# Kernel optimization log

Hardware: AMD Instinct MI355X
Metric: run time of the kernel (lower is better)

## Reference

```python
import jax, jax.numpy as jnp
import numpy as np

TEMPERATURE = 4.0

def setup_inputs() -> dict:
    key = jax.random.key(0)
    k1, k2 = jax.random.split(key)
    query = jax.random.normal(k1, (128, 128, 256), dtype=jnp.float32)      # (B, D, Q)
    context = jax.random.normal(k2, (128, 128, 32, 32), dtype=jnp.float32)  # (B, D, H, W)
    return {"query": query, "context": context}

def reference(query, context):
    B, D, Q = query.shape
    H, W = context.shape[2], context.shape[3]
    L = H * W  # context_length
    context_flat = context.reshape(B, D, L)                    # (B, D, L)
    # scores[b, l, q] = sum_d context[b, d, l] * query[b, d, q]
    scores = jnp.einsum('bdl,bdq->blq', context_flat, query)   # (B, L, Q)
    # first softmax: over query dim (context -> query)
    attn_q = jax.nn.softmax(scores, axis=-1)                   # (B, L, Q)
    # second softmax: over context dim with temperature (query -> context)
    attn_c = jax.nn.softmax(attn_q.transpose(0, 2, 1) * TEMPERATURE, axis=-1)  # (B, Q, L)
    # weighted_context[b, d, q] = sum_l context[b, d, l] * attn_c[b, q, l]
    weighted_context = jnp.einsum('bdl,bql->bdq', context_flat, attn_c)  # (B, D, Q)
    attention_map = attn_c.reshape(B, Q, H, W)
    return (weighted_context, attention_map)
```

## Files before the change

kernel.cpp:

```cpp
#include <hip/hip_runtime.h>
#include <math.h>

#define B_ 128
#define D_ 128
#define Q_ 256
#define L_ 1024

typedef __attribute__((ext_vector_type(8))) short s16x8;
typedef __attribute__((ext_vector_type(4))) float f32x4;

__device__ __forceinline__ unsigned short f2bf(float x) {
  unsigned u = __float_as_uint(x);
  u += 0x7FFF + ((u >> 16) & 1);
  return (unsigned short)(u >> 16);
}
__device__ __forceinline__ float bf2f(unsigned short h) {
  return __uint_as_float(((unsigned)h) << 16);
}
__device__ __forceinline__ uint2 pack4bf(float4 v) {
  uint2 r;
  r.x = ((unsigned)f2bf(v.y) << 16) | (unsigned)f2bf(v.x);
  r.y = ((unsigned)f2bf(v.w) << 16) | (unsigned)f2bf(v.z);
  return r;
}
__device__ __forceinline__ void split8(const float* x, s16x8& hi, s16x8& lo) {
#pragma unroll
  for (int j = 0; j < 8; j++) {
    unsigned short h = f2bf(x[j]);
    hi[j] = (short)h;
    lo[j] = (short)f2bf(x[j] - bf2f(h));
  }
}

__global__ __launch_bounds__(256, 2) void k1_attnq(
    const float* __restrict__ query, const float* __restrict__ ctx,
    float* __restrict__ attq, float* __restrict__ pd) {
  __shared__ float sm[4][64], ss[4][64], fm[64], fs[64];
  const int lt = blockIdx.x, b = blockIdx.y;
  const int l0 = lt * 64;
  const int tid = threadIdx.x;
  const int wq = tid >> 6;
  const int lane = tid & 63, quad = lane >> 4, l15 = lane & 15;

  const float* Qb = query + (size_t)b * D_ * Q_;
  const float* Cb = ctx + (size_t)b * D_ * L_ + l0;

  f32x4 acc[4][4];
#pragma unroll
  for (int mi = 0; mi < 4; mi++)
#pragma unroll
    for (int ni = 0; ni < 4; ni++) acc[mi][ni] = (f32x4){0.f, 0.f, 0.f, 0.f};

#pragma unroll 2
  for (int k0 = 0; k0 < D_; k0 += 32) {
    const int kq = k0 + quad * 8;
    s16x8 ah[4], al[4], bh[4], bl[4];
#pragma unroll
    for (int mi = 0; mi < 4; mi++) {
      const float* p = Qb + (size_t)kq * Q_ + wq * 64 + mi * 16 + l15;
      float x[8];
#pragma unroll
      for (int j = 0; j < 8; j++) x[j] = p[(size_t)j * Q_];
      split8(x, ah[mi], al[mi]);
    }
#pragma unroll
    for (int ni = 0; ni < 4; ni++) {
      const float* p = Cb + (size_t)kq * L_ + ni * 16 + l15;
      float x[8];
#pragma unroll
      for (int j = 0; j < 8; j++) x[j] = p[(size_t)j * L_];
      split8(x, bh[ni], bl[ni]);
    }
#pragma unroll
    for (int mi = 0; mi < 4; mi++)
#pragma unroll
      for (int ni = 0; ni < 4; ni++) {
        acc[mi][ni] = __builtin_amdgcn_mfma_f32_16x16x32_bf16(
            ah[mi], bh[ni], acc[mi][ni], 0, 0, 0);
        acc[mi][ni] = __builtin_amdgcn_mfma_f32_16x16x32_bf16(
            ah[mi], bl[ni], acc[mi][ni], 0, 0, 0);
        acc[mi][ni] = __builtin_amdgcn_mfma_f32_16x16x32_bf16(
            al[mi], bh[ni], acc[mi][ni], 0, 0, 0);
      }
  }

#pragma unroll
  for (int ni = 0; ni < 4; ni++) {
    float m = -1e30f;
#pragma unroll
    for (int mi = 0; mi < 4; mi++)
#pragma unroll
      for (int r = 0; r < 4; r++) m = fmaxf(m, acc[mi][ni][r]);
    m = fmaxf(m, __shfl_xor(m, 16));
    m = fmaxf(m, __shfl_xor(m, 32));
    float s = 0.f;
#pragma unroll
    for (int mi = 0; mi < 4; mi++)
#pragma unroll
      for (int r = 0; r < 4; r++) s += __expf(acc[mi][ni][r] - m);
    s += __shfl_xor(s, 16);
    s += __shfl_xor(s, 32);
    if (quad == 0) {
      sm[wq][ni * 16 + l15] = m;
      ss[wq][ni * 16 + l15] = s;
    }
  }
  __syncthreads();
  if (tid < 64) {
    float m0 = sm[0][tid], m1 = sm[1][tid], m2 = sm[2][tid], m3 = sm[3][tid];
    float M = fmaxf(fmaxf(m0, m1), fmaxf(m2, m3));
    float S = ss[0][tid] * __expf(m0 - M) + ss[1][tid] * __expf(m1 - M) +
              ss[2][tid] * __expf(m2 - M) + ss[3][tid] * __expf(m3 - M);
    fm[tid] = M;
    fs[tid] = 1.f / S;
  }
  __syncthreads();

  float fmv[4], fiv[4];
#pragma unroll
  for (int ni = 0; ni < 4; ni++) {
    fmv[ni] = fm[ni * 16 + l15];
    fiv[ni] = fs[ni * 16 + l15];
  }
  float* Ab = attq + ((size_t)b * Q_ + wq * 64) * L_ + l0;
  float dsum[4][4];
#pragma unroll
  for (int mi = 0; mi < 4; mi++)
#pragma unroll
    for (int r = 0; r < 4; r++) dsum[mi][r] = 0.f;
#pragma unroll
  for (int mi = 0; mi < 4; mi++)
#pragma unroll
    for (int r = 0; r < 4; r++) {
      const int q = mi * 16 + quad * 4 + r;
#pragma unroll
      for (int ni = 0; ni < 4; ni++) {
        float a = __expf(acc[mi][ni][r] - fmv[ni]) * fiv[ni];
        Ab[(size_t)q * L_ + ni * 16 + l15] = a;
        dsum[mi][r] += __expf(4.f * a);
      }
    }
#pragma unroll
  for (int mi = 0; mi < 4; mi++)
#pragma unroll
    for (int r = 0; r < 4; r++) {
      float v = dsum[mi][r];
      v += __shfl_xor(v, 1);
      v += __shfl_xor(v, 2);
      v += __shfl_xor(v, 4);
      v += __shfl_xor(v, 8);
      dsum[mi][r] = v;
    }
  if (l15 == 0) {
#pragma unroll
    for (int mi = 0; mi < 4; mi++)
#pragma unroll
      for (int r = 0; r < 4; r++)
        pd[(size_t)lt * (B_ * Q_) + b * Q_ + wq * 64 + mi * 16 + quad * 4 +
           r] = dsum[mi][r];
  }
}

__global__ __launch_bounds__(256) void k2_invd(const float* __restrict__ pd,
                                               float* __restrict__ invd) {
  const int i = blockIdx.x * 256 + threadIdx.x;
  float s = 0.f;
#pragma unroll
  for (int t = 0; t < 16; t++) s += pd[(size_t)t * (B_ * Q_) + i];
  invd[i] = 1.f / s;
}

__global__ __launch_bounds__(256) void k4_weighted(
    const float* __restrict__ ctx, float* __restrict__ attn,
    const float* __restrict__ invd, float* __restrict__ W) {
  __shared__ unsigned short As[128][32];
  __shared__ unsigned short Bs[64][32];
  const int b = blockIdx.y, q0 = blockIdx.x * 64;
  const int tid = threadIdx.x;
  const int w = tid >> 6, lane = tid & 63, quad = lane >> 4, l15 = lane & 15;
  const int wd = (w >> 1) * 64, wn = (w & 1) * 32;

  const float* Cb = ctx + (size_t)b * D_ * L_;
  float* Ab = attn + ((size_t)b * Q_ + q0) * L_;

  const int lc = (tid & 7) * 4;
  const int rr = tid >> 3;
  const float id0 = invd[b * Q_ + q0 + rr];
  const float id1 = invd[b * Q_ + q0 + rr + 32];

  f32x4 acc[4][2];
#pragma unroll
  for (int mi = 0; mi < 4; mi++)
#pragma unroll
    for (int ni = 0; ni < 2; ni++) acc[mi][ni] = (f32x4){0.f, 0.f, 0.f, 0.f};

  for (int l0 = 0; l0 < L_; l0 += 32) {
    if (l0) __syncthreads();
#pragma unroll
    for (int h = 0; h < 4; h++) {
      const int d = rr + h * 32;
      float4 cv = *(const float4*)(Cb + (size_t)d * L_ + l0 + lc);
      *(uint2*)&As[d][lc] = pack4bf(cv);
    }
#pragma unroll
    for (int h = 0; h < 2; h++) {
      const int q = rr + h * 32;
      float* p = Ab + (size_t)q * L_ + l0 + lc;
      float4 a = *(const float4*)p;
      const float idv = h ? id1 : id0;
      float4 t;
      t.x = __expf(4.f * a.x) * idv;
      t.y = __expf(4.f * a.y) * idv;
      t.z = __expf(4.f * a.z) * idv;
      t.w = __expf(4.f * a.w) * idv;
      *(float4*)p = t;
      *(uint2*)&Bs[q][lc] = pack4bf(t);
    }
    __syncthreads();

    s16x8 af[4], bq[2];
#pragma unroll
    for (int mi = 0; mi < 4; mi++)
      af[mi] = *(const s16x8*)&As[wd + mi * 16 + l15][quad * 8];
#pragma unroll
    for (int ni = 0; ni < 2; ni++)
      bq[ni] = *(const s16x8*)&Bs[wn + ni * 16 + l15][quad * 8];
#pragma unroll
    for (int mi = 0; mi < 4; mi++)
#pragma unroll
      for (int ni = 0; ni < 2; ni++)
        acc[mi][ni] = __builtin_amdgcn_mfma_f32_16x16x32_bf16(
            af[mi], bq[ni], acc[mi][ni], 0, 0, 0);
  }

  float* Wb = W + (size_t)b * D_ * Q_;
#pragma unroll
  for (int mi = 0; mi < 4; mi++)
#pragma unroll
    for (int ni = 0; ni < 2; ni++)
#pragma unroll
      for (int r = 0; r < 4; r++)
        Wb[(size_t)(wd + mi * 16 + quad * 4 + r) * Q_ + q0 + wn + ni * 16 +
           l15] = acc[mi][ni][r];
}

extern "C" void kernel_launch(void* const* d_in, const int* in_sizes, int n_in,
                              void* d_out, int out_size, void* d_ws,
                              size_t ws_size, hipStream_t stream) {
  const float* query = (const float*)d_in[0];
  const float* ctx = (const float*)d_in[1];
  float* W = (float*)d_out;
  float* attn = (float*)d_out + (size_t)B_ * D_ * Q_;

  const size_t need = (size_t)17 * B_ * Q_ * sizeof(float);
  float* pd = (ws_size >= need && d_ws) ? (float*)d_ws : W;
  float* invd = pd + (size_t)16 * B_ * Q_;

  k1_attnq<<<dim3(L_ / 64, B_), 256, 0, stream>>>(query, ctx, attn, pd);
  k2_invd<<<dim3(B_ * Q_ / 256), 256, 0, stream>>>(pd, invd);
  k4_weighted<<<dim3(Q_ / 64, B_), 256, 0, stream>>>(ctx, attn, invd, W);
}
```

Measured before the change: 316.8 us.

## Pre-split inputs to bf16 hi/lo layout and store intermediate attention in fp16

Adds a pre-pass that transposes query and context into K-contiguous bf16 hi/lo arrays, staged in the output buffers. The score kernel can then load MFMA fragments with vector loads instead of strided scalar loads and skip the per-block split. The first-softmax result now goes to an fp16 workspace instead of an fp32 read-modify-write of the attention map, which reduces traffic in the weighted-sum kernel. The trade-offs are an extra launch, a large workspace requirement that falls back to the old path if unmet, and lower precision in the intermediate attention values.

```diff
diff --git a/kernel.cpp b/kernel.cpp
--- a/kernel.cpp
+++ b/kernel.cpp
@@ -5,9 +5,12 @@
 #define D_ 128
 #define Q_ 256
 #define L_ 1024
+#define BQ_ ((size_t)B_ * Q_)
+#define BQL_ ((size_t)B_ * Q_ * L_)
 
 typedef __attribute__((ext_vector_type(8))) short s16x8;
 typedef __attribute__((ext_vector_type(4))) float f32x4;
+typedef __attribute__((ext_vector_type(8))) _Float16 f16x8;
 
 __device__ __forceinline__ unsigned short f2bf(float x) {
   unsigned u = __float_as_uint(x);
@@ -32,7 +35,189 @@
   }
 }
 
-__global__ __launch_bounds__(256, 2) void k1_attnq(
+__global__ __launch_bounds__(256) void p1_split(
+    const float* __restrict__ query, const float* __restrict__ ctx,
+    unsigned short* __restrict__ Qs, unsigned short* __restrict__ Cs) {
+  __shared__ float T[128][132];
+  const int b = blockIdx.y;
+  const int xt = blockIdx.x;
+  const float* src;
+  unsigned short* dst;
+  int C, c0;
+  if (xt < 2) {
+    src = query + (size_t)b * D_ * Q_;
+    dst = Qs + (size_t)b * Q_ * 256;
+    C = Q_;
+    c0 = xt * 128;
+  } else {
+    src = ctx + (size_t)b * D_ * L_;
+    dst = Cs + (size_t)b * L_ * 256;
+    C = L_;
+    c0 = (xt - 2) * 128;
+  }
+  const int t = threadIdx.x;
+  const int col4 = (t & 31) * 4, kr = t >> 5;
+#pragma unroll
+  for (int i = 0; i < 16; i++) {
+    const int k = kr + i * 8;
+    *(float4*)&T[k][col4] = *(const float4*)(src + (size_t)k * C + c0 + col4);
+  }
+  __syncthreads();
+  const int q = t >> 1, half = t & 1;
+  unsigned short* drow = dst + (size_t)(c0 + q) * 256;
+#pragma unroll
+  for (int g = 0; g < 8; g++) {
+    const int k0 = half * 64 + g * 8;
+    float x[8];
+#pragma unroll
+    for (int j = 0; j < 8; j++) x[j] = T[k0 + j][q];
+    uint4 vh, vl;
+    unsigned hh[8], ll[8];
+#pragma unroll
+    for (int j = 0; j < 8; j++) {
+      unsigned short h = f2bf(x[j]);
+      hh[j] = h;
+      ll[j] = f2bf(x[j] - bf2f(h));
+    }
+    vh.x = hh[0] | (hh[1] << 16);
+    vh.y = hh[2] | (hh[3] << 16);
+    vh.z = hh[4] | (hh[5] << 16);
+    vh.w = hh[6] | (hh[7] << 16);
+    vl.x = ll[0] | (ll[1] << 16);
+    vl.y = ll[2] | (ll[3] << 16);
+    vl.z = ll[4] | (ll[5] << 16);
+    vl.w = ll[6] | (ll[7] << 16);
+    *(uint4*)&drow[k0] = vh;
+    *(uint4*)&drow[128 + k0] = vl;
+  }
+}
+
+template <bool F16>
+__global__ __launch_bounds__(256) void k1_fast(
+    const unsigned short* __restrict__ Qs, const unsigned short* __restrict__ Cs,
+    void* __restrict__ attq, float* __restrict__ pd) {
+  __shared__ float sm[4][64], ss[4][64], fm[64], fs[64];
+  const int lt = blockIdx.x, b = blockIdx.y;
+  const int l0 = lt * 64;
+  const int tid = threadIdx.x;
+  const int wq = tid >> 6;
+  const int lane = tid & 63, quad = lane >> 4, l15 = lane & 15;
+
+  const unsigned short* Qb = Qs + (size_t)b * Q_ * 256;
+  const unsigned short* Cb = Cs + (size_t)b * L_ * 256;
+
+  f32x4 acc[4][4];
+#pragma unroll
+  for (int mi = 0; mi < 4; mi++)
+#pragma unroll
+    for (int ni = 0; ni < 4; ni++) acc[mi][ni] = (f32x4){0.f, 0.f, 0.f, 0.f};
+
+#pragma unroll 2
+  for (int k0 = 0; k0 < D_; k0 += 32) {
+    s16x8 ah[4], al[4], bh[4], bl[4];
+#pragma unroll
+    for (int mi = 0; mi < 4; mi++) {
+      const unsigned short* p =
+          Qb + (size_t)(wq * 64 + mi * 16 + l15) * 256 + k0 + quad * 8;
+      ah[mi] = *(const s16x8*)p;
+      al[mi] = *(const s16x8*)(p + 128);
+    }
+#pragma unroll
+    for (int ni = 0; ni < 4; ni++) {
+      const unsigned short* p =
+          Cb + (size_t)(l0 + ni * 16 + l15) * 256 + k0 + quad * 8;
+      bh[ni] = *(const s16x8*)p;
+      bl[ni] = *(const s16x8*)(p + 128);
+    }
+#pragma unroll
+    for (int mi = 0; mi < 4; mi++)
+#pragma unroll
+      for (int ni = 0; ni < 4; ni++) {
+        acc[mi][ni] = __builtin_amdgcn_mfma_f32_16x16x32_bf16(
+            ah[mi], bh[ni], acc[mi][ni], 0, 0, 0);
+        acc[mi][ni] = __builtin_amdgcn_mfma_f32_16x16x32_bf16(
+            ah[mi], bl[ni], acc[mi][ni], 0, 0, 0);
+        acc[mi][ni] = __builtin_amdgcn_mfma_f32_16x16x32_bf16(
+            al[mi], bh[ni], acc[mi][ni], 0, 0, 0);
+      }
+  }
+
+#pragma unroll
+  for (int ni = 0; ni < 4; ni++) {
+    float m = -1e30f;
+#pragma unroll
+    for (int mi = 0; mi < 4; mi++)
+#pragma unroll
+      for (int r = 0; r < 4; r++) m = fmaxf(m, acc[mi][ni][r]);
+    m = fmaxf(m, __shfl_xor(m, 16));
+    m = fmaxf(m, __shfl_xor(m, 32));
+    float s = 0.f;
+#pragma unroll
+    for (int mi = 0; mi < 4; mi++)
+#pragma unroll
+      for (int r = 0; r < 4; r++) s += __expf(acc[mi][ni][r] - m);
+    s += __shfl_xor(s, 16);
+    s += __shfl_xor(s, 32);
+    if (quad == 0) {
+      sm[wq][ni * 16 + l15] = m;
+      ss[wq][ni * 16 + l15] = s;
+    }
+  }
+  __syncthreads();
+  if (tid < 64) {
+    float m0 = sm[0][tid], m1 = sm[1][tid], m2 = sm[2][tid], m3 = sm[3][tid];
+    float M = fmaxf(fmaxf(m0, m1), fmaxf(m2, m3));
+    float S = ss[0][tid] * __expf(m0 - M) + ss[1][tid] * __expf(m1 - M) +
+              ss[2][tid] * __expf(m2 - M) + ss[3][tid] * __expf(m3 - M);
+    fm[tid] = M;
+    fs[tid] = 1.f / S;
+  }
+  __syncthreads();
+
+  float fmv[4], fiv[4];
+#pragma unroll
+  for (int ni = 0; ni < 4; ni++) {
+    fmv[ni] = fm[ni * 16 + l15];
+    fiv[ni] = fs[ni * 16 + l15];
+  }
+  float dsum[4][4];
+#pragma unroll
+  for (int mi = 0; mi < 4; mi++)
+#pragma unroll
+    for (int r = 0; r < 4; r++) dsum[mi][r] = 0.f;
+
+  const size_t rowbase = ((size_t)b * Q_ + wq * 64) * L_ + l0;
+#pragma unroll
+  for (int mi = 0; mi < 4; mi++)
+#pragma unroll
+    for (int r = 0; r < 4; r++) {
+      const int q = mi * 16 + quad * 4 + r;
+#pragma unroll
+      for (int ni = 0; ni < 4; ni++) {
+        float a = __expf(acc[mi][ni][r] - fmv[ni]) * fiv[ni];
+        if (F16)
+          ((_Float16*)attq)[rowbase + (size_t)q * L_ + ni * 16 + l15] =
+              (_Float16)a;
+        else
+          ((float*)attq)[rowbase + (size_t)q * L_ + ni * 16 + l15] = a;
+        dsum[mi][r] += __expf(4.f * a);
+      }
+    }
+#pragma unroll
+  for (int mi = 0; mi < 4; mi++)
+#pragma unroll
+    for (int r = 0; r < 4; r++) {
+      float v = dsum[mi][r];
+      v += __shfl_xor(v, 1);
+      v += __shfl_xor(v, 2);
+      v += __shfl_xor(v, 4);
+      v += __shfl_xor(v, 8);
+      if (l15 == 0)
+        pd[(size_t)lt * BQ_ + b * Q_ + wq * 64 + mi * 16 + quad * 4 + r] = v;
+    }
+}
+
+__global__ __launch_bounds__(256, 2) void k1_slow(
     const float* __restrict__ query, const float* __restrict__ ctx,
     float* __restrict__ attq, float* __restrict__ pd) {
   __shared__ float sm[4][64], ss[4][64], fm[64], fs[64];
@@ -149,16 +334,9 @@
       v += __shfl_xor(v, 2);
       v += __shfl_xor(v, 4);
       v += __shfl_xor(v, 8);
-      dsum[mi][r] = v;
-    }
-  if (l15 == 0) {
-#pragma unroll
-    for (int mi = 0; mi < 4; mi++)
-#pragma unroll
-      for (int r = 0; r < 4; r++)
-        pd[(size_t)lt * (B_ * Q_) + b * Q_ + wq * 64 + mi * 16 + quad * 4 +
-           r] = dsum[mi][r];
-  }
+      if (l15 == 0)
+        pd[(size_t)lt * BQ_ + b * Q_ + wq * 64 + mi * 16 + quad * 4 + r] = v;
+    }
 }
 
 __global__ __launch_bounds__(256) void k2_invd(const float* __restrict__ pd,
@@ -166,13 +344,15 @@
   const int i = blockIdx.x * 256 + threadIdx.x;
   float s = 0.f;
 #pragma unroll
-  for (int t = 0; t < 16; t++) s += pd[(size_t)t * (B_ * Q_) + i];
+  for (int t = 0; t < 16; t++) s += pd[(size_t)t * BQ_ + i];
   invd[i] = 1.f / s;
 }
 
+template <bool F16>
 __global__ __launch_bounds__(256) void k4_weighted(
-    const float* __restrict__ ctx, float* __restrict__ attn,
-    const float* __restrict__ invd, float* __restrict__ W) {
+    const float* __restrict__ ctx, const void* __restrict__ attn,
+    float* __restrict__ map, const float* __restrict__ invd,
+    float* __restrict__ W) {
   __shared__ unsigned short As[128][32];
   __shared__ unsigned short Bs[64][32];
   const int b = blockIdx.y, q0 = blockIdx.x * 64;
@@ -181,12 +361,16 @@
   const int wd = (w >> 1) * 64, wn = (w & 1) * 32;
 
   const float* Cb = ctx + (size_t)b * D_ * L_;
-  float* Ab = attn + ((size_t)b * Q_ + q0) * L_;
-
-  const int lc = (tid & 7) * 4;
-  const int rr = tid >> 3;
-  const float id0 = invd[b * Q_ + q0 + rr];
-  const float id1 = invd[b * Q_ + q0 + rr + 32];
+  const int lc = (tid & 7) * 4, rr = tid >> 3;
+
+  const int qv = tid >> 2, lc8 = (tid & 3) * 8;
+  float idv = 0.f, id0 = 0.f, id1 = 0.f;
+  if (F16) {
+    idv = invd[b * Q_ + q0 + qv];
+  } else {
+    id0 = invd[b * Q_ + q0 + rr];
+    id1 = invd[b * Q_ + q0 + rr + 32];
+  }
 
   f32x4 acc[4][2];
 #pragma unroll
@@ -202,19 +386,37 @@
       float4 cv = *(const float4*)(Cb + (size_t)d * L_ + l0 + lc);
       *(uint2*)&As[d][lc] = pack4bf(cv);
     }
-#pragma unroll
-    for (int h = 0; h < 2; h++) {
-      const int q = rr + h * 32;
-      float* p = Ab + (size_t)q * L_ + l0 + lc;
-      float4 a = *(const float4*)p;
-      const float idv = h ? id1 : id0;
-      float4 t;
-      t.x = __expf(4.f * a.x) * idv;
-      t.y = __expf(4.f * a.y) * idv;
-      t.z = __expf(4.f * a.z) * idv;
-      t.w = __expf(4.f * a.w) * idv;
-      *(float4*)p = t;
-      *(uint2*)&Bs[q][lc] = pack4bf(t);
+    if (F16) {
+      const _Float16* Arow =
+          (const _Float16*)attn + ((size_t)b * Q_ + q0 + qv) * L_ + l0 + lc8;
+      f16x8 av = *(const f16x8*)Arow;
+      float t[8];
+#pragma unroll
+      for (int j = 0; j < 8; j++) t[j] = __expf(4.f * (float)av[j]) * idv;
+      float* Mrow = map + ((size_t)b * Q_ + q0 + qv) * L_ + l0 + lc8;
+      *(float4*)Mrow = make_float4(t[0], t[1], t[2], t[3]);
+      *(float4*)(Mrow + 4) = make_float4(t[4], t[5], t[6], t[7]);
+      uint4 pk;
+      pk.x = (unsigned)f2bf(t[0]) | ((unsigned)f2bf(t[1]) << 16);
+      pk.y = (unsigned)f2bf(t[2]) | ((unsigned)f2bf(t[3]) << 16);
+      pk.z = (unsigned)f2bf(t[4]) | ((unsigned)f2bf(t[5]) << 16);
+      pk.w = (unsigned)f2bf(t[6]) | ((unsigned)f2bf(t[7]) << 16);
+      *(uint4*)&Bs[qv][lc8] = pk;
+    } else {
+#pragma unroll
+      for (int h = 0; h < 2; h++) {
+        const int q = rr + h * 32;
+        float* p = map + ((size_t)b * Q_ + q0 + q) * L_ + l0 + lc;
+        float4 a = *(const float4*)p;
+        const float iv = h ? id1 : id0;
+        float4 t;
+        t.x = __expf(4.f * a.x) * iv;
+        t.y = __expf(4.f * a.y) * iv;
+        t.z = __expf(4.f * a.z) * iv;
+        t.w = __expf(4.f * a.w) * iv;
+        *(float4*)p = t;
+        *(uint2*)&Bs[q][lc] = pack4bf(t);
+      }
     }
     __syncthreads();
 
@@ -250,13 +452,28 @@
   const float* query = (const float*)d_in[0];
   const float* ctx = (const float*)d_in[1];
   float* W = (float*)d_out;
-  float* attn = (float*)d_out + (size_t)B_ * D_ * Q_;
-
-  const size_t need = (size_t)17 * B_ * Q_ * sizeof(float);
-  float* pd = (ws_size >= need && d_ws) ? (float*)d_ws : W;
-  float* invd = pd + (size_t)16 * B_ * Q_;
-
-  k1_attnq<<<dim3(L_ / 64, B_), 256, 0, stream>>>(query, ctx, attn, pd);
-  k2_invd<<<dim3(B_ * Q_ / 256), 256, 0, stream>>>(pd, invd);
-  k4_weighted<<<dim3(Q_ / 64, B_), 256, 0, stream>>>(ctx, attn, invd, W);
-}
+  float* map = (float*)d_out + (size_t)B_ * D_ * Q_;
+
+  const size_t need_fast = BQL_ * 2 + 17 * BQ_ * 4;
+  if (ws_size >= need_fast && d_ws) {
+    _Float16* attn16 = (_Float16*)d_ws;
+    float* pd = (float*)((char*)d_ws + BQL_ * 2);
+    float* invd = pd + 16 * BQ_;
+    unsigned short* Qs = (unsigned short*)W;
+    unsigned short* Cs = (unsigned short*)map;
+
+    p1_split<<<dim3(10, B_), 256, 0, stream>>>(query, ctx, Qs, Cs);
+    k1_fast<true><<<dim3(L_ / 64, B_), 256, 0, stream>>>(Qs, Cs, attn16, pd);
+    k2_invd<<<dim3(BQ_ / 256), 256, 0, stream>>>(pd, invd);
+    k4_weighted<true><<<dim3(Q_ / 64, B_), 256, 0, stream>>>(ctx, attn16, map,
+                                                             invd, W);
+  } else {
+    const size_t need_pd = 17 * BQ_ * 4;
+    float* pd = (ws_size >= need_pd && d_ws) ? (float*)d_ws : W;
+    float* invd = pd + 16 * BQ_;
+    k1_slow<<<dim3(L_ / 64, B_), 256, 0, stream>>>(query, ctx, map, pd);
+    k2_invd<<<dim3(BQ_ / 256), 256, 0, stream>>>(pd, invd);
+    k4_weighted<false><<<dim3(Q_ / 64, B_), 256, 0, stream>>>(ctx, map, map,
+                                                              invd, W);
+  }
+}
```

New measurement: 397.1 us. 25.3% more time.

## Pre-split query to bf16 hi/lo once and prefetch operands in GEMM loops

Applied to the files above, without the earlier changes.

Adds a kernel that transposes the query and splits it into bf16 high/low halves once per batch, stored temporarily in the output W buffer. The scores kernel then loads these with vector loads instead of redoing strided fp32 loads and splitting in every L-tile block. Context loads in the scores kernel and ctx/map loads in the weighted kernel are register double-buffered to overlap global latency with MFMA work. This costs an extra launch and a 16 MB intermediate write/read, and the small-workspace fallback now aliases pd onto the map buffer.

```diff
diff --git a/kernel.cpp b/kernel.cpp
--- a/kernel.cpp
+++ b/kernel.cpp
@@ -5,6 +5,7 @@
 #define D_ 128
 #define Q_ 256
 #define L_ 1024
+#define BQ_ ((size_t)B_ * Q_)
 
 typedef __attribute__((ext_vector_type(8))) short s16x8;
 typedef __attribute__((ext_vector_type(4))) float f32x4;
@@ -32,8 +33,48 @@
   }
 }
 
-__global__ __launch_bounds__(256, 2) void k1_attnq(
-    const float* __restrict__ query, const float* __restrict__ ctx,
+__global__ __launch_bounds__(256) void p1q_split(
+    const float* __restrict__ query, unsigned short* __restrict__ Qs) {
+  __shared__ float T[128][132];
+  const int b = blockIdx.y, c0 = blockIdx.x * 128;
+  const float* src = query + (size_t)b * D_ * Q_;
+  const int t = threadIdx.x;
+  const int col4 = (t & 31) * 4, kr = t >> 5;
+#pragma unroll
+  for (int i = 0; i < 16; i++) {
+    const int k = kr + i * 8;
+    *(float4*)&T[k][col4] = *(const float4*)(src + (size_t)k * Q_ + c0 + col4);
+  }
+  __syncthreads();
+  const int q = t >> 1, half = t & 1;
+  unsigned short* drow = Qs + (size_t)(b * Q_ + c0 + q) * 256;
+#pragma unroll
+  for (int g = 0; g < 8; g++) {
+    const int k0 = half * 64 + g * 8;
+    unsigned hh[8], ll[8];
+#pragma unroll
+    for (int j = 0; j < 8; j++) {
+      float x = T[k0 + j][q];
+      unsigned short h = f2bf(x);
+      hh[j] = h;
+      ll[j] = f2bf(x - bf2f(h));
+    }
+    uint4 vh, vl;
+    vh.x = hh[0] | (hh[1] << 16);
+    vh.y = hh[2] | (hh[3] << 16);
+    vh.z = hh[4] | (hh[5] << 16);
+    vh.w = hh[6] | (hh[7] << 16);
+    vl.x = ll[0] | (ll[1] << 16);
+    vl.y = ll[2] | (ll[3] << 16);
+    vl.z = ll[4] | (ll[5] << 16);
+    vl.w = ll[6] | (ll[7] << 16);
+    *(uint4*)&drow[k0] = vh;
+    *(uint4*)&drow[128 + k0] = vl;
+  }
+}
+
+__global__ __launch_bounds__(256, 2) void k1_mid(
+    const unsigned short* __restrict__ Qs, const float* __restrict__ ctx,
     float* __restrict__ attq, float* __restrict__ pd) {
   __shared__ float sm[4][64], ss[4][64], fm[64], fs[64];
   const int lt = blockIdx.x, b = blockIdx.y;
@@ -42,7 +83,7 @@
   const int wq = tid >> 6;
   const int lane = tid & 63, quad = lane >> 4, l15 = lane & 15;
 
-  const float* Qb = query + (size_t)b * D_ * Q_;
+  const unsigned short* Qb = Qs + (size_t)b * Q_ * 256;
   const float* Cb = ctx + (size_t)b * D_ * L_ + l0;
 
   f32x4 acc[4][4];
@@ -51,26 +92,37 @@
 #pragma unroll
     for (int ni = 0; ni < 4; ni++) acc[mi][ni] = (f32x4){0.f, 0.f, 0.f, 0.f};
 
-#pragma unroll 2
-  for (int k0 = 0; k0 < D_; k0 += 32) {
-    const int kq = k0 + quad * 8;
-    s16x8 ah[4], al[4], bh[4], bl[4];
+  float xb[2][4][8];
+#pragma unroll
+  for (int ni = 0; ni < 4; ni++) {
+    const float* p = Cb + (size_t)(quad * 8) * L_ + ni * 16 + l15;
+#pragma unroll
+    for (int j = 0; j < 8; j++) xb[0][ni][j] = p[(size_t)j * L_];
+  }
+
+#pragma unroll
+  for (int c = 0; c < 4; c++) {
+    const int k0 = c * 32;
+    const int cur = c & 1, nxt = cur ^ 1;
+    s16x8 ah[4], al[4];
 #pragma unroll
     for (int mi = 0; mi < 4; mi++) {
-      const float* p = Qb + (size_t)kq * Q_ + wq * 64 + mi * 16 + l15;
-      float x[8];
-#pragma unroll
-      for (int j = 0; j < 8; j++) x[j] = p[(size_t)j * Q_];
-      split8(x, ah[mi], al[mi]);
-    }
-#pragma unroll
-    for (int ni = 0; ni < 4; ni++) {
-      const float* p = Cb + (size_t)kq * L_ + ni * 16 + l15;
-      float x[8];
-#pragma unroll
-      for (int j = 0; j < 8; j++) x[j] = p[(size_t)j * L_];
-      split8(x, bh[ni], bl[ni]);
-    }
+      const unsigned short* p =
+          Qb + (size_t)(wq * 64 + mi * 16 + l15) * 256 + k0 + quad * 8;
+      ah[mi] = *(const s16x8*)p;
+      al[mi] = *(const s16x8*)(p + 128);
+    }
+    if (c < 3) {
+#pragma unroll
+      for (int ni = 0; ni < 4; ni++) {
+        const float* p = Cb + (size_t)(k0 + 32 + quad * 8) * L_ + ni * 16 + l15;
+#pragma unroll
+        for (int j = 0; j < 8; j++) xb[nxt][ni][j] = p[(size_t)j * L_];
+      }
+    }
+    s16x8 bh[4], bl[4];
+#pragma unroll
+    for (int ni = 0; ni < 4; ni++) split8(xb[cur][ni], bh[ni], bl[ni]);
 #pragma unroll
     for (int mi = 0; mi < 4; mi++)
 #pragma unroll
@@ -149,16 +201,9 @@
       v += __shfl_xor(v, 2);
       v += __shfl_xor(v, 4);
       v += __shfl_xor(v, 8);
-      dsum[mi][r] = v;
-    }
-  if (l15 == 0) {
-#pragma unroll
-    for (int mi = 0; mi < 4; mi++)
-#pragma unroll
-      for (int r = 0; r < 4; r++)
-        pd[(size_t)lt * (B_ * Q_) + b * Q_ + wq * 64 + mi * 16 + quad * 4 +
-           r] = dsum[mi][r];
-  }
+      if (l15 == 0)
+        pd[(size_t)lt * BQ_ + b * Q_ + wq * 64 + mi * 16 + quad * 4 + r] = v;
+    }
 }
 
 __global__ __launch_bounds__(256) void k2_invd(const float* __restrict__ pd,
@@ -166,12 +211,12 @@
   const int i = blockIdx.x * 256 + threadIdx.x;
   float s = 0.f;
 #pragma unroll
-  for (int t = 0; t < 16; t++) s += pd[(size_t)t * (B_ * Q_) + i];
+  for (int t = 0; t < 16; t++) s += pd[(size_t)t * BQ_ + i];
   invd[i] = 1.f / s;
 }
 
 __global__ __launch_bounds__(256) void k4_weighted(
-    const float* __restrict__ ctx, float* __restrict__ attn,
+    const float* __restrict__ ctx, float* __restrict__ map,
     const float* __restrict__ invd, float* __restrict__ W) {
   __shared__ unsigned short As[128][32];
   __shared__ unsigned short Bs[64][32];
@@ -181,10 +226,7 @@
   const int wd = (w >> 1) * 64, wn = (w & 1) * 32;
 
   const float* Cb = ctx + (size_t)b * D_ * L_;
-  float* Ab = attn + ((size_t)b * Q_ + q0) * L_;
-
-  const int lc = (tid & 7) * 4;
-  const int rr = tid >> 3;
+  const int lc = (tid & 7) * 4, rr = tid >> 3;
   const float id0 = invd[b * Q_ + q0 + rr];
   const float id1 = invd[b * Q_ + q0 + rr + 32];
 
@@ -194,29 +236,43 @@
 #pragma unroll
     for (int ni = 0; ni < 2; ni++) acc[mi][ni] = (f32x4){0.f, 0.f, 0.f, 0.f};
 
+  float4 cva[4], ava[2];
+#pragma unroll
+  for (int h = 0; h < 4; h++)
+    cva[h] = *(const float4*)(Cb + (size_t)(rr + h * 32) * L_ + lc);
+#pragma unroll
+  for (int h = 0; h < 2; h++)
+    ava[h] =
+        *(const float4*)(map + ((size_t)b * Q_ + q0 + rr + h * 32) * L_ + lc);
+
   for (int l0 = 0; l0 < L_; l0 += 32) {
     if (l0) __syncthreads();
 #pragma unroll
-    for (int h = 0; h < 4; h++) {
-      const int d = rr + h * 32;
-      float4 cv = *(const float4*)(Cb + (size_t)d * L_ + l0 + lc);
-      *(uint2*)&As[d][lc] = pack4bf(cv);
-    }
+    for (int h = 0; h < 4; h++) *(uint2*)&As[rr + h * 32][lc] = pack4bf(cva[h]);
 #pragma unroll
     for (int h = 0; h < 2; h++) {
       const int q = rr + h * 32;
-      float* p = Ab + (size_t)q * L_ + l0 + lc;
-      float4 a = *(const float4*)p;
-      const float idv = h ? id1 : id0;
+      const float iv = h ? id1 : id0;
       float4 t;
-      t.x = __expf(4.f * a.x) * idv;
-      t.y = __expf(4.f * a.y) * idv;
-      t.z = __expf(4.f * a.z) * idv;
-      t.w = __expf(4.f * a.w) * idv;
-      *(float4*)p = t;
+      t.x = __expf(4.f * ava[h].x) * iv;
+      t.y = __expf(4.f * ava[h].y) * iv;
+      t.z = __expf(4.f * ava[h].z) * iv;
+      t.w = __expf(4.f * ava[h].w) * iv;
+      *(float4*)(map + ((size_t)b * Q_ + q0 + q) * L_ + l0 + lc) = t;
       *(uint2*)&Bs[q][lc] = pack4bf(t);
     }
     __syncthreads();
+
+    if (l0 + 32 < L_) {
+#pragma unroll
+      for (int h = 0; h < 4; h++)
+        cva[h] =
+            *(const float4*)(Cb + (size_t)(rr + h * 32) * L_ + l0 + 32 + lc);
+#pragma unroll
+      for (int h = 0; h < 2; h++)
+        ava[h] = *(const float4*)(map + ((size_t)b * Q_ + q0 + rr + h * 32) *
+                                            L_ + l0 + 32 + lc);
+    }
 
     s16x8 af[4], bq[2];
 #pragma unroll
@@ -250,13 +306,15 @@
   const float* query = (const float*)d_in[0];
   const float* ctx = (const float*)d_in[1];
   float* W = (float*)d_out;
-  float* attn = (float*)d_out + (size_t)B_ * D_ * Q_;
-
-  const size_t need = (size_t)17 * B_ * Q_ * sizeof(float);
-  float* pd = (ws_size >= need && d_ws) ? (float*)d_ws : W;
-  float* invd = pd + (size_t)16 * B_ * Q_;
-
-  k1_attnq<<<dim3(L_ / 64, B_), 256, 0, stream>>>(query, ctx, attn, pd);
-  k2_invd<<<dim3(B_ * Q_ / 256), 256, 0, stream>>>(pd, invd);
-  k4_weighted<<<dim3(Q_ / 64, B_), 256, 0, stream>>>(ctx, attn, invd, W);
-}
+  float* map = (float*)d_out + (size_t)B_ * D_ * Q_;
+  unsigned short* Qs = (unsigned short*)W;
+
+  const size_t need_pd = 17 * BQ_ * sizeof(float);
+  float* pd = (ws_size >= need_pd && d_ws) ? (float*)d_ws : map;
+  float* invd = pd + 16 * BQ_;
+
+  p1q_split<<<dim3(2, B_), 256, 0, stream>>>(query, Qs);
+  k1_mid<<<dim3(L_ / 64, B_), 256, 0, stream>>>(Qs, ctx, map, pd);
+  k2_invd<<<dim3(BQ_ / 256), 256, 0, stream>>>(pd, invd);
+  k4_weighted<<<dim3(Q_ / 64, B_), 256, 0, stream>>>(ctx, map, invd, W);
+}
```

Result: slower. 349.4 us (+10.3%).
